# Optimization experiments

Measured on AMD Instinct MI355X. Metric: run time of the kernel, lower is better.

## Reference

```python
import math
import jax, jax.numpy as jnp
from jax import lax
import numpy as np

L, B, S, D, H, F = 12, 8, 512, 768, 12, 3072
DH = D // H
REL_POS_BINS, MAX_REL_POS = 32, 128
REL_2D_POS_BINS, MAX_REL_2D_POS = 64, 256
LN_EPS = 1e-12


def _rel_bucket(rel, num_buckets, max_distance):
    # bidirectional relative_position_bucket as in LayoutLMv2
    num_buckets = num_buckets // 2
    ret = (rel > 0).astype(jnp.int32) * num_buckets
    n = jnp.abs(rel)
    max_exact = num_buckets // 2
    is_small = n < max_exact
    n_safe = jnp.maximum(n, 1)  # avoid log(0); masked by is_small anyway
    val_if_large = max_exact + (
        jnp.log(n_safe.astype(jnp.float32) / max_exact)
        / math.log(max_distance / max_exact) * (num_buckets - max_exact)
    ).astype(jnp.int32)
    val_if_large = jnp.minimum(val_if_large, num_buckets - 1)
    return ret + jnp.where(is_small, n.astype(jnp.int32), val_if_large)


def _layernorm(x, g, b):
    mu = jnp.mean(x, axis=-1, keepdims=True)
    var = jnp.var(x, axis=-1, keepdims=True)
    return (x - mu) * lax.rsqrt(var + LN_EPS) * g + b


def _encoder(hidden_states, attention_mask, position_ids, bbox,
             qkv_w, q_bias, v_bias, attn_out_w, attn_out_b, ln1_g, ln1_b,
             inter_w, inter_b, ffn_out_w, ffn_out_b, ln2_g, ln2_b,
             rel_pos_table, rel_x_table, rel_y_table):
    b, s, d = hidden_states.shape
    h = rel_pos_table.shape[1]
    dh = d // h
    # 1D relative position bias: [B,H,S,S]
    rel = position_ids[:, None, :] - position_ids[:, :, None]  # [B,S,S], rel[b,i,j]=p[j]-p[i]
    rp = _rel_bucket(rel, REL_POS_BINS, MAX_REL_POS)
    bias = jnp.transpose(rel_pos_table[rp], (0, 3, 1, 2))
    # 2D spatial bias from bbox x (coord 0) and y (coord 3)
    cx = bbox[:, :, 0]
    cy = bbox[:, :, 3]
    bx = _rel_bucket(cx[:, None, :] - cx[:, :, None], REL_2D_POS_BINS, MAX_REL_2D_POS)
    by = _rel_bucket(cy[:, None, :] - cy[:, :, None], REL_2D_POS_BINS, MAX_REL_2D_POS)
    bias = bias + jnp.transpose(rel_x_table[bx] + rel_y_table[by], (0, 3, 1, 2))
    mask = attention_mask.astype(bool)  # [B,1,1,S], True = masked
    inv_sqrt_dh = 1.0 / math.sqrt(dh)

    def layer(carry, p):
        (qw, qb, vb, aow, aob, g1, b1, iw, ib, fow, fob, g2, b2) = p
        qkv = carry @ qw                      # [B,S,3D] (fast_qkv, no bias)
        q, k, v = jnp.split(qkv, 3, axis=-1)
        q = (q + qb) * inv_sqrt_dh
        v = v + vb
        q = q.reshape(b, s, h, dh)
        k = k.reshape(b, s, h, dh)
        v = v.reshape(b, s, h, dh)
        scores = jnp.einsum('bihd,bjhd->bhij', q, k) + bias
        scores = jnp.where(mask, -jnp.inf, scores.astype(jnp.float32))
        probs = jax.nn.softmax(scores, axis=-1).astype(carry.dtype)
        ctx = jnp.einsum('bhij,bjhd->bihd', probs, v).reshape(b, s, d)
        attn = _layernorm(ctx @ aow + aob + carry, g1, b1)
        ff = jax.nn.gelu(attn @ iw + ib, approximate=False)
        out = _layernorm(ff @ fow + fob + attn, g2, b2)
        return out, None

    params = (qkv_w, q_bias, v_bias, attn_out_w, attn_out_b, ln1_g, ln1_b,
              inter_w, inter_b, ffn_out_w, ffn_out_b, ln2_g, ln2_b)
    out, _ = lax.scan(layer, hidden_states, params)
    return out


def setup_inputs() -> dict:
    key = jax.random.key(0)
    ks = jax.random.split(key, 12)
    w = 0.02
    inp = {
        'hidden_states': jax.random.normal(ks[0], (B, S, D), jnp.float32),
        'attention_mask': jax.random.randint(ks[1], (B, 1, 1, S), 0, 2).astype(jnp.int32),
        'position_ids': jnp.broadcast_to(jnp.arange(S, dtype=jnp.int64), (B, S)),
        'bbox': jax.random.randint(ks[2], (B, S, 4), 0, 1000).astype(jnp.int64),
        'qkv_w': jax.random.normal(ks[3], (L, D, 3 * D), jnp.float32) * w,
        'q_bias': jnp.zeros((L, D), jnp.float32),
        'v_bias': jnp.zeros((L, D), jnp.float32),
        'attn_out_w': jax.random.normal(ks[4], (L, D, D), jnp.float32) * w,
        'attn_out_b': jnp.zeros((L, D), jnp.float32),
        'ln1_g': jnp.ones((L, D), jnp.float32),
        'ln1_b': jnp.zeros((L, D), jnp.float32),
        'inter_w': jax.random.normal(ks[5], (L, D, F), jnp.float32) * w,
        'inter_b': jnp.zeros((L, F), jnp.float32),
        'ffn_out_w': jax.random.normal(ks[6], (L, F, D), jnp.float32) * w,
        'ffn_out_b': jnp.zeros((L, D), jnp.float32),
        'ln2_g': jnp.ones((L, D), jnp.float32),
        'ln2_b': jnp.zeros((L, D), jnp.float32),
        'rel_pos_table': jax.random.normal(ks[7], (REL_POS_BINS, H), jnp.float32) * w,
        'rel_x_table': jax.random.normal(ks[8], (REL_2D_POS_BINS, H), jnp.float32) * w,
        'rel_y_table': jax.random.normal(ks[9], (REL_2D_POS_BINS, H), jnp.float32) * w,
    }
    return inp


def reference(hidden_states, attention_mask, position_ids, bbox,
              qkv_w, q_bias, v_bias, attn_out_w, attn_out_b, ln1_g, ln1_b,
              inter_w, inter_b, ffn_out_w, ffn_out_b, ln2_g, ln2_b,
              rel_pos_table, rel_x_table, rel_y_table):
    return _encoder(hidden_states, attention_mask, position_ids, bbox,
                    qkv_w, q_bias, v_bias, attn_out_w, attn_out_b, ln1_g, ln1_b,
                    inter_w, inter_b, ffn_out_w, ffn_out_b, ln2_g, ln2_b,
                    rel_pos_table, rel_x_table, rel_y_table)
```

## Files before the change

### kernel.cpp

```cpp
#include <hip/hip_runtime.h>
#include <hip/hip_bf16.h>
#include <cstdint>

#define LCONST 12
#define BCONST 8
#define SCONST 512
#define DCONST 768
#define HCONST 12
#define FCONST 3072
#define DH 64

typedef __bf16 bf16x8 __attribute__((ext_vector_type(8)));
typedef float f32x4 __attribute__((ext_vector_type(4)));

__device__ __forceinline__ void gload16(const void* g, void* l) {
    __builtin_amdgcn_global_load_lds(
            (const __attribute__((address_space(1))) void*)g,
            (__attribute__((address_space(3))) void*)l, 16, 0, 0);
}

__device__ __forceinline__ int rbucket(int rel, int nb2, int maxex) {
    int ret = (rel > 0) ? nb2 : 0;
    int n = (rel < 0) ? -rel : rel;
    if (n < maxex) return ret + n;
    const float inv_ln16 = 0.36067376022224085f;
    int v = maxex + (int)(logf((float)n / (float)maxex) * inv_ln16 * (float)(nb2 - maxex));
    if (v > nb2 - 1) v = nb2 - 1;
    return ret + v;
}

__global__ __launch_bounds__(256) void build_idx_kernel(
        const int* __restrict__ pos, const int* __restrict__ bbox,
        int* __restrict__ idx) {
    size_t t = (size_t)blockIdx.x * 256 + threadIdx.x;
    int j = (int)(t & 511);
    int i = (int)((t >> 9) & 511);
    int b = (int)(t >> 18);
    int rp = rbucket(pos[b * SCONST + j] - pos[b * SCONST + i], 16, 8);
    int cxi = bbox[((size_t)b * SCONST + i) * 4 + 0];
    int cxj = bbox[((size_t)b * SCONST + j) * 4 + 0];
    int cyi = bbox[((size_t)b * SCONST + i) * 4 + 3];
    int cyj = bbox[((size_t)b * SCONST + j) * 4 + 3];
    int bx = rbucket(cxj - cxi, 32, 16);
    int by = rbucket(cyj - cyi, 32, 16);
    idx[t] = rp | (bx << 5) | (by << 11);
}

__global__ __launch_bounds__(256) void cvt_kernel(const float* __restrict__ in,
                                                  __bf16* __restrict__ out, int n) {
    int t = blockIdx.x * 256 + threadIdx.x;
    if (t < n) out[t] = (__bf16)in[t];
}

__global__ __launch_bounds__(256) void transpose_cvt_kernel(
        const float* __restrict__ in, __bf16* __restrict__ out, int R, int C) {
    __shared__ float tile[32][33];
    size_t off = (size_t)blockIdx.y * R * C;
    int nct = C >> 5;
    int c0 = (blockIdx.x % nct) << 5;
    int r0 = (blockIdx.x / nct) << 5;
    int tx = threadIdx.x & 31, ty = threadIdx.x >> 5;
#pragma unroll
    for (int i = 0; i < 32; i += 8)
        tile[ty + i][tx] = in[off + (size_t)(r0 + ty + i) * C + c0 + tx];
    __syncthreads();
#pragma unroll
    for (int i = 0; i < 32; i += 8)
        out[off + (size_t)(c0 + ty + i) * R + r0 + tx] = (__bf16)tile[tx][ty + i];
}

template <int MODE>
__global__ __launch_bounds__(256) void gemm_kernel(
        const __bf16* __restrict__ A, const __bf16* __restrict__ Bt,
        int M, int N, int K,
        const float* __restrict__ cbias, const float* __restrict__ vbias,
        const float* __restrict__ resid, float* __restrict__ outF,
        __bf16* __restrict__ outQ, __bf16* __restrict__ outK,
        __bf16* __restrict__ outV, __bf16* __restrict__ outB) {
    __shared__ __align__(16) __bf16 As[128 * 32];
    __shared__ __align__(16) __bf16 Bs[128 * 32];
    int tid = threadIdx.x;
    int wid = tid >> 6, lane = tid & 63, quad = lane >> 4, l16 = lane & 15;
    int nTM = M >> 7;
    int tileM = (blockIdx.x % nTM) << 7;
    int tileN = (blockIdx.x / nTM) << 7;
    int wm = wid >> 1, wn = wid & 1;

    const __bf16* gA0 = A + (size_t)(tileM + wid * 32 + (lane >> 2)) * K + ((lane & 3) << 3);
    const __bf16* gB0 = Bt + (size_t)(tileN + wid * 32 + (lane >> 2)) * K + ((lane & 3) << 3);
    __bf16* lA0 = As + wid * 1024;
    __bf16* lB0 = Bs + wid * 1024;

    f32x4 acc[4][4] = {};

    for (int k0 = 0; k0 < K; k0 += 32) {
        gload16(gA0 + k0, lA0);
        gload16(gA0 + (size_t)16 * K + k0, lA0 + 512);
        gload16(gB0 + k0, lB0);
        gload16(gB0 + (size_t)16 * K + k0, lB0 + 512);
        __syncthreads();
        bf16x8 af[4], bfr[4];
#pragma unroll
        for (int mt = 0; mt < 4; mt++)
            af[mt] = *(const bf16x8*)&As[(wm * 64 + mt * 16 + l16) * 32 + quad * 8];
#pragma unroll
        for (int nt = 0; nt < 4; nt++)
            bfr[nt] = *(const bf16x8*)&Bs[(wn * 64 + nt * 16 + l16) * 32 + quad * 8];
#pragma unroll
        for (int mt = 0; mt < 4; mt++)
#pragma unroll
            for (int nt = 0; nt < 4; nt++)
                acc[mt][nt] = __builtin_amdgcn_mfma_f32_16x16x32_bf16(
                        af[mt], bfr[nt], acc[mt][nt], 0, 0, 0);
        __syncthreads();
    }

#pragma unroll
    for (int mt = 0; mt < 4; mt++)
#pragma unroll
        for (int nt = 0; nt < 4; nt++)
#pragma unroll
            for (int r = 0; r < 4; r++) {
                int row = tileM + wm * 64 + mt * 16 + quad * 4 + r;
                int col = tileN + wn * 64 + nt * 16 + l16;
                float v = acc[mt][nt][r];
                if (MODE == 0) {
                    int b = row >> 9, s = row & 511;
                    if (col < 768) {
                        int h = col >> 6, dh = col & 63;
                        float q = (v + cbias[col]) * 0.125f;
                        outQ[(((size_t)b * HCONST + h) * SCONST + s) * DH + dh] = (__bf16)q;
                    } else if (col < 1536) {
                        int c2 = col - 768;
                        int h = c2 >> 6, dh = c2 & 63;
                        outK[(((size_t)b * HCONST + h) * SCONST + s) * DH + dh] = (__bf16)v;
                    } else {
                        int c2 = col - 1536;
                        int h = c2 >> 6, dh = c2 & 63;
                        float vv = v + vbias[c2];
                        outV[(((size_t)b * HCONST + h) * DH + dh) * SCONST + s] = (__bf16)vv;
                    }
                } else if (MODE == 1 || MODE == 3) {
                    size_t o = (size_t)row * N + col;
                    outF[o] = v + cbias[col] + resid[o];
                } else {
                    float u = v + cbias[col];
                    float g = 0.5f * u * (1.0f + erff(u * 0.70710678118654752f));
                    outB[(size_t)row * N + col] = (__bf16)g;
                }
            }
}

__global__ __launch_bounds__(256) void attn_kernel(
        const __bf16* __restrict__ qbuf, const __bf16* __restrict__ kbuf,
        const __bf16* __restrict__ vbuf, const int* __restrict__ idx,
        const int* __restrict__ amask, const float* __restrict__ tpg,
        const float* __restrict__ txg, const float* __restrict__ tyg,
        __bf16* __restrict__ ctx) {
    int bh = blockIdx.x >> 3;
    int i0 = (blockIdx.x & 7) << 6;
    int b = bh / HCONST, h = bh % HCONST;

    __shared__ __align__(16) __bf16 Ks[64 * 64];
    __shared__ __align__(16) __bf16 Vs[64 * 64];
    __shared__ __align__(16) __bf16 Ps[4][16 * 64];
    __shared__ float tp[32], tx[64], ty[64];
    __shared__ float mk[512];

    int tid = threadIdx.x;
    if (tid < 32) tp[tid] = tpg[tid * HCONST + h];
    if (tid < 64) {
        tx[tid] = txg[tid * HCONST + h];
        ty[tid] = tyg[tid * HCONST + h];
    }
    for (int j = tid; j < 512; j += 256)
        mk[j] = amask[b * SCONST + j] ? -INFINITY : 0.0f;

    int wid = tid >> 6, lane = tid & 63, quad = lane >> 4, l16 = lane & 15;

    const __bf16* qrow = qbuf + ((size_t)bh * SCONST + i0 + wid * 16 + l16) * DH;
    bf16x8 qf0 = *(const bf16x8*)(qrow + quad * 8);
    bf16x8 qf1 = *(const bf16x8*)(qrow + 32 + quad * 8);

    const __bf16* kg = kbuf + (size_t)bh * SCONST * DH;
    const __bf16* vg = vbuf + (size_t)bh * DH * SCONST;

    f32x4 O[4] = {};
    float m_r[4] = {-1e30f, -1e30f, -1e30f, -1e30f};
    float l_r[4] = {0.f, 0.f, 0.f, 0.f};

    __syncthreads();

    for (int j0 = 0; j0 < SCONST; j0 += 64) {
        {
            const __bf16* kbase = kg + (size_t)j0 * DH;
#pragma unroll
            for (int s = 0; s < 2; s++) {
                int c = wid * 2 + s;
                gload16(kbase + c * 512 + lane * 8, Ks + c * 512);
                int dh = c * 8 + (lane >> 3), cc = lane & 7;
                gload16(vg + (size_t)dh * SCONST + j0 + cc * 8, Vs + c * 512);
            }
        }
        __syncthreads();

        float sc[4][4];
#pragma unroll
        for (int jt = 0; jt < 4; jt++) {
            f32x4 a = {};
            bf16x8 kf0 = *(const bf16x8*)&Ks[(jt * 16 + l16) * 64 + quad * 8];
            bf16x8 kf1 = *(const bf16x8*)&Ks[(jt * 16 + l16) * 64 + 32 + quad * 8];
            a = __builtin_amdgcn_mfma_f32_16x16x32_bf16(qf0, kf0, a, 0, 0, 0);
            a = __builtin_amdgcn_mfma_f32_16x16x32_bf16(qf1, kf1, a, 0, 0, 0);
#pragma unroll
            for (int r = 0; r < 4; r++) {
                int i = i0 + wid * 16 + quad * 4 + r;
                int j = j0 + jt * 16 + l16;
                int pk = idx[((size_t)b * SCONST + i) * SCONST + j];
                float bias = tp[pk & 31] + tx[(pk >> 5) & 63] + ty[(pk >> 11) & 63];
                sc[jt][r] = a[r] + bias + mk[j];
            }
        }

        float p[4][4];
#pragma unroll
        for (int r = 0; r < 4; r++) {
            float mb = fmaxf(fmaxf(sc[0][r], sc[1][r]), fmaxf(sc[2][r], sc[3][r]));
#pragma unroll
            for (int m = 1; m < 16; m <<= 1) mb = fmaxf(mb, __shfl_xor(mb, m, 64));
            float mn = fmaxf(m_r[r], mb);
            float alpha = __expf(m_r[r] - mn);
            m_r[r] = mn;
            float ls = 0.f;
#pragma unroll
            for (int jt = 0; jt < 4; jt++) {
                float pv = __expf(sc[jt][r] - mn);
                p[jt][r] = pv;
                ls += pv;
            }
#pragma unroll
            for (int m = 1; m < 16; m <<= 1) ls += __shfl_xor(ls, m, 64);
            l_r[r] = l_r[r] * alpha + ls;
#pragma unroll
            for (int nt = 0; nt < 4; nt++) O[nt][r] *= alpha;
        }

        __bf16* pl = &Ps[wid][0];
#pragma unroll
        for (int jt = 0; jt < 4; jt++)
#pragma unroll
            for (int r = 0; r < 4; r++)
                pl[(quad * 4 + r) * 64 + jt * 16 + l16] = (__bf16)p[jt][r];

        bf16x8 pa0 = *(const bf16x8*)&pl[l16 * 64 + quad * 8];
        bf16x8 pa1 = *(const bf16x8*)&pl[l16 * 64 + 32 + quad * 8];
#pragma unroll
        for (int nt = 0; nt < 4; nt++) {
            bf16x8 vb0 = *(const bf16x8*)&Vs[(nt * 16 + l16) * 64 + quad * 8];
            bf16x8 vb1 = *(const bf16x8*)&Vs[(nt * 16 + l16) * 64 + 32 + quad * 8];
            O[nt] = __builtin_amdgcn_mfma_f32_16x16x32_bf16(pa0, vb0, O[nt], 0, 0, 0);
            O[nt] = __builtin_amdgcn_mfma_f32_16x16x32_bf16(pa1, vb1, O[nt], 0, 0, 0);
        }
        __syncthreads();
    }

#pragma unroll
    for (int nt = 0; nt < 4; nt++)
#pragma unroll
        for (int r = 0; r < 4; r++) {
            int i = i0 + wid * 16 + quad * 4 + r;
            int dh = nt * 16 + l16;
            float o = O[nt][r] / l_r[r];
            ctx[((size_t)b * SCONST + i) * DCONST + h * DH + dh] = (__bf16)o;
        }
}

__global__ __launch_bounds__(256) void ln_kernel(
        const float* __restrict__ in, const float* __restrict__ g,
        const float* __restrict__ bb, float* __restrict__ outF,
        __bf16* __restrict__ outB) {
    __shared__ float red[4];
    int row = blockIdx.x, t = threadIdx.x;
    const float* x = in + (size_t)row * DCONST;
    float v0 = x[t], v1 = x[t + 256], v2 = x[t + 512];
    float s = v0 + v1 + v2;
#pragma unroll
    for (int m = 1; m < 64; m <<= 1) s += __shfl_xor(s, m, 64);
    if ((t & 63) == 0) red[t >> 6] = s;
    __syncthreads();
    s = red[0] + red[1] + red[2] + red[3];
    __syncthreads();
    float mu = s * (1.0f / 768.0f);
    float d0 = v0 - mu, d1 = v1 - mu, d2 = v2 - mu;
    float q = d0 * d0 + d1 * d1 + d2 * d2;
#pragma unroll
    for (int m = 1; m < 64; m <<= 1) q += __shfl_xor(q, m, 64);
    if ((t & 63) == 0) red[t >> 6] = q;
    __syncthreads();
    q = red[0] + red[1] + red[2] + red[3];
    float rstd = rsqrtf(q * (1.0f / 768.0f) + 1e-12f);
    float y0 = d0 * rstd * g[t] + bb[t];
    float y1 = d1 * rstd * g[t + 256] + bb[t + 256];
    float y2 = d2 * rstd * g[t + 512] + bb[t + 512];
    size_t o = (size_t)row * DCONST;
    outF[o + t] = y0;
    outF[o + t + 256] = y1;
    outF[o + t + 512] = y2;
    outB[o + t] = (__bf16)y0;
    outB[o + t + 256] = (__bf16)y1;
    outB[o + t + 512] = (__bf16)y2;
}

extern "C" void kernel_launch(void* const* d_in, const int* in_sizes, int n_in,
                              void* d_out, int out_size, void* d_ws, size_t ws_size,
                              hipStream_t stream) {
    const float* hidden = (const float*)d_in[0];
    const int* amask = (const int*)d_in[1];
    const int* pos = (const int*)d_in[2];
    const int* bbox = (const int*)d_in[3];
    const float* qkv_w = (const float*)d_in[4];
    const float* q_bias = (const float*)d_in[5];
    const float* v_bias = (const float*)d_in[6];
    const float* aow = (const float*)d_in[7];
    const float* aob = (const float*)d_in[8];
    const float* ln1g = (const float*)d_in[9];
    const float* ln1b = (const float*)d_in[10];
    const float* iw = (const float*)d_in[11];
    const float* ib = (const float*)d_in[12];
    const float* fow = (const float*)d_in[13];
    const float* fob = (const float*)d_in[14];
    const float* ln2g = (const float*)d_in[15];
    const float* ln2b = (const float*)d_in[16];
    const float* tpt = (const float*)d_in[17];
    const float* txt = (const float*)d_in[18];
    const float* tyt = (const float*)d_in[19];
    float* out = (float*)d_out;

    char* w = (char*)d_ws;
    size_t used = 0;
    auto carve = [&](size_t bytes) {
        char* p = w + used;
        used += (bytes + 255) & ~(size_t)255;
        return p;
    };
    const size_t MT = 4096;
    __bf16* qbuf = (__bf16*)carve(MT * 768 * 2);
    __bf16* kbuf = (__bf16*)carve(MT * 768 * 2);
    __bf16* vbuf = (__bf16*)carve(MT * 768 * 2);
    __bf16* xbf = (__bf16*)carve(MT * 768 * 2);
    __bf16* ctxbf = (__bf16*)carve(MT * 768 * 2);
    float* attnf = (float*)carve(MT * 768 * 4);
    __bf16* attnbf = (__bf16*)carve(MT * 768 * 2);
    __bf16* ffbf = (__bf16*)carve(MT * 3072 * 2);
    float* t1 = (float*)carve(MT * 768 * 4);
    int* idxb = (int*)carve((size_t)BCONST * SCONST * SCONST * 4);

    const size_t wq_sz = (size_t)2304 * 768 * 2;
    const size_t wa_sz = (size_t)768 * 768 * 2;
    const size_t wi_sz = (size_t)3072 * 768 * 2;
    const size_t wf_sz = (size_t)768 * 3072 * 2;
    const size_t wsum = wq_sz + wa_sz + wi_sz + wf_sz;
    bool full = (ws_size >= used + 12 * wsum + (12 * 4 + 4) * 256);
    int nlw = full ? 12 : 1;
    __bf16* wqT = (__bf16*)carve(wq_sz * nlw);
    __bf16* waT = (__bf16*)carve(wa_sz * nlw);
    __bf16* wiT = (__bf16*)carve(wi_sz * nlw);
    __bf16* wfT = (__bf16*)carve(wf_sz * nlw);

    build_idx_kernel<<<(BCONST * SCONST * SCONST) / 256, 256, 0, stream>>>(pos, bbox, idxb);
    cvt_kernel<<<(int)(MT * 768 / 256), 256, 0, stream>>>(hidden, xbf, (int)(MT * 768));

    if (full) {
        transpose_cvt_kernel<<<dim3((2304 / 32) * (768 / 32), 12), 256, 0, stream>>>(
                qkv_w, wqT, 768, 2304);
        transpose_cvt_kernel<<<dim3((768 / 32) * (768 / 32), 12), 256, 0, stream>>>(
                aow, waT, 768, 768);
        transpose_cvt_kernel<<<dim3((3072 / 32) * (768 / 32), 12), 256, 0, stream>>>(
                iw, wiT, 768, 3072);
        transpose_cvt_kernel<<<dim3((768 / 32) * (3072 / 32), 12), 256, 0, stream>>>(
                fow, wfT, 3072, 768);
    }

    for (int l = 0; l < LCONST; l++) {
        __bf16* wq_l = wqT + (full ? (size_t)l * 2304 * 768 : 0);
        __bf16* wa_l = waT + (full ? (size_t)l * 768 * 768 : 0);
        __bf16* wi_l = wiT + (full ? (size_t)l * 3072 * 768 : 0);
        __bf16* wf_l = wfT + (full ? (size_t)l * 768 * 3072 : 0);
        if (!full) {
            transpose_cvt_kernel<<<dim3((2304 / 32) * (768 / 32), 1), 256, 0, stream>>>(
                    qkv_w + (size_t)l * 768 * 2304, wq_l, 768, 2304);
            transpose_cvt_kernel<<<dim3((768 / 32) * (768 / 32), 1), 256, 0, stream>>>(
                    aow + (size_t)l * 768 * 768, wa_l, 768, 768);
            transpose_cvt_kernel<<<dim3((3072 / 32) * (768 / 32), 1), 256, 0, stream>>>(
                    iw + (size_t)l * 768 * 3072, wi_l, 768, 3072);
            transpose_cvt_kernel<<<dim3((768 / 32) * (3072 / 32), 1), 256, 0, stream>>>(
                    fow + (size_t)l * 3072 * 768, wf_l, 3072, 768);
        }

        gemm_kernel<0><<<(4096 / 128) * (2304 / 128), 256, 0, stream>>>(
                xbf, wq_l, 4096, 2304, 768, q_bias + (size_t)l * 768,
                v_bias + (size_t)l * 768, nullptr, nullptr, qbuf, kbuf, vbuf, nullptr);

        attn_kernel<<<BCONST * HCONST * (SCONST / 64), 256, 0, stream>>>(
                qbuf, kbuf, vbuf, idxb, amask, tpt, txt, tyt, ctxbf);

        const float* xres = (l == 0) ? hidden : out;
        gemm_kernel<1><<<(4096 / 128) * (768 / 128), 256, 0, stream>>>(
                ctxbf, wa_l, 4096, 768, 768, aob + (size_t)l * 768, nullptr, xres, t1,
                nullptr, nullptr, nullptr, nullptr);
        ln_kernel<<<4096, 256, 0, stream>>>(t1, ln1g + (size_t)l * 768,
                                            ln1b + (size_t)l * 768, attnf, attnbf);

        gemm_kernel<2><<<(4096 / 128) * (3072 / 128), 256, 0, stream>>>(
                attnbf, wi_l, 4096, 3072, 768, ib + (size_t)l * 3072, nullptr, nullptr,
                nullptr, nullptr, nullptr, nullptr, ffbf);

        gemm_kernel<3><<<(4096 / 128) * (768 / 128), 256, 0, stream>>>(
                ffbf, wf_l, 4096, 768, 3072, fob + (size_t)l * 768, nullptr, attnf, t1,
                nullptr, nullptr, nullptr, nullptr);
        ln_kernel<<<4096, 256, 0, stream>>>(t1, ln2g + (size_t)l * 768,
                                            ln2b + (size_t)l * 768, out, xbf);
    }
}
```

Measured before the change: 3.298 ms.

## Split-K the N=768 GEMMs into four partials and reduce inside layernorm

The attention-output and FFN-output GEMMs (N=768) only launch 192 tiles, which underfills the GPU's compute units. They now split K into four chunks over a second grid dimension and write fp32 partial sums to a scratch buffer. The layernorm kernel sums the four partials, adds bias and residual, then normalizes. This adds extra fp32 traffic: four partial writes and reads per element instead of one.

```diff
diff --git a/kernel.cpp b/kernel.cpp
--- a/kernel.cpp
+++ b/kernel.cpp
@@ -72,9 +72,9 @@
 template <int MODE>
 __global__ __launch_bounds__(256) void gemm_kernel(
         const __bf16* __restrict__ A, const __bf16* __restrict__ Bt,
-        int M, int N, int K,
+        int M, int N, int Kc, int ldK,
         const float* __restrict__ cbias, const float* __restrict__ vbias,
-        const float* __restrict__ resid, float* __restrict__ outF,
+        float* __restrict__ part,
         __bf16* __restrict__ outQ, __bf16* __restrict__ outK,
         __bf16* __restrict__ outV, __bf16* __restrict__ outB) {
     __shared__ __align__(16) __bf16 As[128 * 32];
@@ -84,20 +84,23 @@
     int nTM = M >> 7;
     int tileM = (blockIdx.x % nTM) << 7;
     int tileN = (blockIdx.x / nTM) << 7;
+    int chunk = blockIdx.y;
     int wm = wid >> 1, wn = wid & 1;
 
-    const __bf16* gA0 = A + (size_t)(tileM + wid * 32 + (lane >> 2)) * K + ((lane & 3) << 3);
-    const __bf16* gB0 = Bt + (size_t)(tileN + wid * 32 + (lane >> 2)) * K + ((lane & 3) << 3);
+    const __bf16* Ab = A + (size_t)chunk * Kc;
+    const __bf16* Bb = Bt + (size_t)chunk * Kc;
+    const __bf16* gA0 = Ab + (size_t)(tileM + wid * 32 + (lane >> 2)) * ldK + ((lane & 3) << 3);
+    const __bf16* gB0 = Bb + (size_t)(tileN + wid * 32 + (lane >> 2)) * ldK + ((lane & 3) << 3);
     __bf16* lA0 = As + wid * 1024;
     __bf16* lB0 = Bs + wid * 1024;
 
     f32x4 acc[4][4] = {};
 
-    for (int k0 = 0; k0 < K; k0 += 32) {
+    for (int k0 = 0; k0 < Kc; k0 += 32) {
         gload16(gA0 + k0, lA0);
-        gload16(gA0 + (size_t)16 * K + k0, lA0 + 512);
+        gload16(gA0 + (size_t)16 * ldK + k0, lA0 + 512);
         gload16(gB0 + k0, lB0);
-        gload16(gB0 + (size_t)16 * K + k0, lB0 + 512);
+        gload16(gB0 + (size_t)16 * ldK + k0, lB0 + 512);
         __syncthreads();
         bf16x8 af[4], bfr[4];
 #pragma unroll
@@ -140,13 +143,12 @@
                         float vv = v + vbias[c2];
                         outV[(((size_t)b * HCONST + h) * DH + dh) * SCONST + s] = (__bf16)vv;
                     }
-                } else if (MODE == 1 || MODE == 3) {
-                    size_t o = (size_t)row * N + col;
-                    outF[o] = v + cbias[col] + resid[o];
-                } else {
+                } else if (MODE == 2) {
                     float u = v + cbias[col];
                     float g = 0.5f * u * (1.0f + erff(u * 0.70710678118654752f));
                     outB[(size_t)row * N + col] = (__bf16)g;
+                } else {
+                    part[(size_t)chunk * M * N + (size_t)row * N + col] = v;
                 }
             }
 }
@@ -275,14 +277,25 @@
         }
 }
 
-__global__ __launch_bounds__(256) void ln_kernel(
-        const float* __restrict__ in, const float* __restrict__ g,
+__global__ __launch_bounds__(256) void ln4_kernel(
+        const float* __restrict__ part, const float* __restrict__ resid,
+        const float* __restrict__ cbias, const float* __restrict__ g,
         const float* __restrict__ bb, float* __restrict__ outF,
         __bf16* __restrict__ outB) {
+    const size_t MN = (size_t)4096 * DCONST;
     __shared__ float red[4];
     int row = blockIdx.x, t = threadIdx.x;
-    const float* x = in + (size_t)row * DCONST;
-    float v0 = x[t], v1 = x[t + 256], v2 = x[t + 512];
+    size_t o = (size_t)row * DCONST;
+    float v0, v1, v2;
+    {
+        int c0 = t, c1 = t + 256, c2 = t + 512;
+        v0 = part[o + c0] + part[MN + o + c0] + part[2 * MN + o + c0] +
+             part[3 * MN + o + c0] + cbias[c0] + resid[o + c0];
+        v1 = part[o + c1] + part[MN + o + c1] + part[2 * MN + o + c1] +
+             part[3 * MN + o + c1] + cbias[c1] + resid[o + c1];
+        v2 = part[o + c2] + part[MN + o + c2] + part[2 * MN + o + c2] +
+             part[3 * MN + o + c2] + cbias[c2] + resid[o + c2];
+    }
     float s = v0 + v1 + v2;
 #pragma unroll
     for (int m = 1; m < 64; m <<= 1) s += __shfl_xor(s, m, 64);
@@ -302,7 +315,6 @@
     float y0 = d0 * rstd * g[t] + bb[t];
     float y1 = d1 * rstd * g[t + 256] + bb[t + 256];
     float y2 = d2 * rstd * g[t + 512] + bb[t + 512];
-    size_t o = (size_t)row * DCONST;
     outF[o + t] = y0;
     outF[o + t + 256] = y1;
     outF[o + t + 512] = y2;
@@ -352,7 +364,7 @@
     float* attnf = (float*)carve(MT * 768 * 4);
     __bf16* attnbf = (__bf16*)carve(MT * 768 * 2);
     __bf16* ffbf = (__bf16*)carve(MT * 3072 * 2);
-    float* t1 = (float*)carve(MT * 768 * 4);
+    float* part = (float*)carve(4 * MT * 768 * 4);
     int* idxb = (int*)carve((size_t)BCONST * SCONST * SCONST * 4);
 
     const size_t wq_sz = (size_t)2304 * 768 * 2;
@@ -397,28 +409,30 @@
                     fow + (size_t)l * 3072 * 768, wf_l, 3072, 768);
         }
 
-        gemm_kernel<0><<<(4096 / 128) * (2304 / 128), 256, 0, stream>>>(
-                xbf, wq_l, 4096, 2304, 768, q_bias + (size_t)l * 768,
-                v_bias + (size_t)l * 768, nullptr, nullptr, qbuf, kbuf, vbuf, nullptr);
+        gemm_kernel<0><<<dim3((4096 / 128) * (2304 / 128), 1), 256, 0, stream>>>(
+                xbf, wq_l, 4096, 2304, 768, 768, q_bias + (size_t)l * 768,
+                v_bias + (size_t)l * 768, nullptr, qbuf, kbuf, vbuf, nullptr);
 
         attn_kernel<<<BCONST * HCONST * (SCONST / 64), 256, 0, stream>>>(
                 qbuf, kbuf, vbuf, idxb, amask, tpt, txt, tyt, ctxbf);
 
+        gemm_kernel<4><<<dim3((4096 / 128) * (768 / 128), 4), 256, 0, stream>>>(
+                ctxbf, wa_l, 4096, 768, 192, 768, nullptr, nullptr, part,
+                nullptr, nullptr, nullptr, nullptr);
         const float* xres = (l == 0) ? hidden : out;
-        gemm_kernel<1><<<(4096 / 128) * (768 / 128), 256, 0, stream>>>(
-                ctxbf, wa_l, 4096, 768, 768, aob + (size_t)l * 768, nullptr, xres, t1,
+        ln4_kernel<<<4096, 256, 0, stream>>>(part, xres, aob + (size_t)l * 768,
+                                             ln1g + (size_t)l * 768,
+                                             ln1b + (size_t)l * 768, attnf, attnbf);
+
+        gemm_kernel<2><<<dim3((4096 / 128) * (3072 / 128), 1), 256, 0, stream>>>(
+                attnbf, wi_l, 4096, 3072, 768, 768, ib + (size_t)l * 3072, nullptr,
+                nullptr, nullptr, nullptr, nullptr, ffbf);
+
+        gemm_kernel<4><<<dim3((4096 / 128) * (768 / 128), 4), 256, 0, stream>>>(
+                ffbf, wf_l, 4096, 768, 768, 3072, nullptr, nullptr, part,
                 nullptr, nullptr, nullptr, nullptr);
-        ln_kernel<<<4096, 256, 0, stream>>>(t1, ln1g + (size_t)l * 768,
-                                            ln1b + (size_t)l * 768, attnf, attnbf);
-
-        gemm_kernel<2><<<(4096 / 128) * (3072 / 128), 256, 0, stream>>>(
-                attnbf, wi_l, 4096, 3072, 768, ib + (size_t)l * 3072, nullptr, nullptr,
-                nullptr, nullptr, nullptr, nullptr, ffbf);
-
-        gemm_kernel<3><<<(4096 / 128) * (768 / 128), 256, 0, stream>>>(
-                ffbf, wf_l, 4096, 768, 3072, fob + (size_t)l * 768, nullptr, attnf, t1,
-                nullptr, nullptr, nullptr, nullptr);
-        ln_kernel<<<4096, 256, 0, stream>>>(t1, ln2g + (size_t)l * 768,
-                                            ln2b + (size_t)l * 768, out, xbf);
-    }
-}
+        ln4_kernel<<<4096, 256, 0, stream>>>(part, attnf, fob + (size_t)l * 768,
+                                             ln2g + (size_t)l * 768,
+                                             ln2b + (size_t)l * 768, out, xbf);
+    }
+}
```

Measured after the change: 2.887 ms. -12.5%, faster.
